# Kernel optimization log

Measured on AMD Instinct MI355X. Metric: run time of the kernel, lower is better.

## Reference

```python
import jax, jax.numpy as jnp
import numpy as np

B, D_FEAT, D_ATTR, N_CLS = 512, 2048, 312, 150


def setup_inputs() -> dict:
    key = jax.random.key(0)
    k1, k2, k3, k4, k5 = jax.random.split(key, 5)
    return {
        "x_f": jax.random.normal(k1, (B, D_FEAT), dtype=jnp.float32),
        "W": jax.random.normal(k2, (D_FEAT, D_ATTR), dtype=jnp.float32) * 0.02,
        "b": jax.random.normal(k3, (D_ATTR,), dtype=jnp.float32) * 0.02,
        "seen_att": jax.random.normal(k4, (N_CLS, D_ATTR), dtype=jnp.float32),
        "x_labels": jax.random.randint(k5, (B,), 0, N_CLS, dtype=jnp.int64),
    }


def reference(x_f, W, b, seen_att, x_labels):
    temp = 1.0
    pre_attr = x_f @ W + b                                # [B, D]
    log_p = jax.nn.log_softmax(pre_attr / temp, axis=-1)  # log pre_attr_softmax
    log_g = jax.nn.log_softmax(seen_att[x_labels] / temp, axis=-1)
    g = jnp.exp(log_g)                                    # gt_attr_softmax [B, D]

    # pairwise KL(target = g_i/g_j || input_logits = log(p_i/p_j)), reduction='sum':
    #   sum_d t * (log t - log_ratio_p)
    t_ratio = g[:, None, :] / g[None, :, :]                               # [B, B, D]
    log_t = log_g[:, None, :] - log_g[None, :, :]                         # [B, B, D]
    log_r = log_p[:, None, :] - log_p[None, :, :]                         # [B, B, D]
    kl = jnp.sum(t_ratio * (log_t - log_r), axis=-1)                      # [B, B]

    same = x_labels[:, None] == x_labels[None, :]
    upper = jnp.triu(jnp.ones((x_labels.shape[0],) * 2, dtype=bool), k=1)
    mask = same & upper

    count = jnp.sum(mask)
    loss = jnp.sum(jnp.where(mask, kl, 0.0))
    return jnp.where(count > 0, loss / count.astype(loss.dtype), loss)
```

## Files before the change

### kernel.cpp

```cpp
#include <hip/hip_runtime.h>
#include <math.h>

#define B      512
#define DF     2048
#define DA     312
#define NTHR   320
#define RT     8
#define KSPLIT 16

__device__ __forceinline__ float wave_max_f(float v) {
  #pragma unroll
  for (int off = 32; off >= 1; off >>= 1)
    v = fmaxf(v, __shfl_down(v, off));
  return v;
}

__device__ __forceinline__ double wave_sum_d(double v) {
  #pragma unroll
  for (int off = 32; off >= 1; off >>= 1)
    v += __shfl_down(v, off);
  return v;
}

__global__ __launch_bounds__(NTHR) void gemm_partial_kernel(
    const float* __restrict__ x_f, const float* __restrict__ W,
    float* __restrict__ part, int KC) {
  const int c    = threadIdx.x;
  const int row0 = blockIdx.x * RT;
  const int k0   = blockIdx.y * KC;

  if (c >= DA) return;

  float acc[RT];
  #pragma unroll
  for (int r = 0; r < RT; ++r) acc[r] = 0.f;

  const float* Wp = W + (size_t)k0 * DA + c;
  const float* xp = x_f + (size_t)row0 * DF + k0;

  for (int k = 0; k < KC; k += 8) {
    float w[8];
    #pragma unroll
    for (int j = 0; j < 8; ++j) w[j] = Wp[(size_t)(k + j) * DA];
    #pragma unroll
    for (int r = 0; r < RT; ++r) {
      const float* xr = xp + (size_t)r * DF + k;
      #pragma unroll
      for (int j = 0; j < 8; ++j) acc[r] = fmaf(xr[j], w[j], acc[r]);
    }
  }

  #pragma unroll
  for (int r = 0; r < RT; ++r)
    part[((size_t)blockIdx.y * B + row0 + r) * DA + c] = acc[r];
}

__global__ __launch_bounds__(NTHR) void row_stats_kernel(
    const float* __restrict__ part, const float* __restrict__ b,
    double* __restrict__ S, int ksplit) {
  __shared__ float  red_f[8];
  __shared__ double red_d[16];
  __shared__ float  bcast_max;

  const int tid  = threadIdx.x;
  const int wid  = tid >> 6;
  const int lane = tid & 63;
  const int row  = blockIdx.x;

  float v = -INFINITY;
  if (tid < DA) {
    float s = b[tid];
    for (int p = 0; p < ksplit; ++p)
      s += part[((size_t)p * B + row) * DA + tid];
    v = s;
  }

  float m = wave_max_f(v);
  if (lane == 0) red_f[wid] = m;
  __syncthreads();
  if (tid == 0) {
    float mm = red_f[0];
    #pragma unroll
    for (int w = 1; w < NTHR / 64; ++w) mm = fmaxf(mm, red_f[w]);
    bcast_max = mm;
  }
  __syncthreads();
  const float rowmax = bcast_max;

  double e  = (tid < DA) ? exp((double)v - (double)rowmax) : 0.0;
  double sp = (tid < DA) ? (double)v : 0.0;
  double es = wave_sum_d(e);
  double ss = wave_sum_d(sp);
  if (lane == 0) { red_d[wid] = es; red_d[8 + wid] = ss; }
  __syncthreads();
  if (tid == 0) {
    double esum = 0.0, ssum = 0.0;
    #pragma unroll
    for (int w = 0; w < NTHR / 64; ++w) { esum += red_d[w]; ssum += red_d[8 + w]; }
    S[row] = ssum - (double)DA * ((double)rowmax + log(esum));
  }
}

__global__ __launch_bounds__(1024) void pair_reduce_kernel(
    const double* __restrict__ S, const int* __restrict__ labels,
    float* __restrict__ out) {
  __shared__ double    Ss[B];
  __shared__ int       Ls[B];
  __shared__ double    red_d[16];
  __shared__ long long red_i[16];

  const int tid = threadIdx.x;
  if (tid < B) { Ss[tid] = S[tid]; Ls[tid] = labels[tid]; }
  __syncthreads();

  double lsum = 0.0;
  long long lcnt = 0;
  for (int p = tid; p < B * B; p += 1024) {
    int i = p >> 9;
    int j = p & (B - 1);
    if (j > i && Ls[i] == Ls[j]) { lsum += Ss[j] - Ss[i]; lcnt++; }
  }

  #pragma unroll
  for (int off = 32; off >= 1; off >>= 1) {
    lsum += __shfl_down(lsum, off);
    lcnt += __shfl_down(lcnt, off);
  }
  const int wid = tid >> 6, lane = tid & 63;
  if (lane == 0) { red_d[wid] = lsum; red_i[wid] = lcnt; }
  __syncthreads();
  if (tid == 0) {
    double s = 0.0; long long c = 0;
    #pragma unroll
    for (int w = 0; w < 16; ++w) { s += red_d[w]; c += red_i[w]; }
    out[0] = (float)((c > 0) ? s / (double)c : s);
  }
}

extern "C" void kernel_launch(void* const* d_in, const int* in_sizes, int n_in,
                              void* d_out, int out_size, void* d_ws, size_t ws_size,
                              hipStream_t stream) {
  const float* x_f    = (const float*)d_in[0];
  const float* W      = (const float*)d_in[1];
  const float* b      = (const float*)d_in[2];
  const int*   labels = (const int*)d_in[4];

  int ksplit = KSPLIT;
  if (ws_size < (size_t)KSPLIT * B * DA * 4 + 8192) ksplit = 2;

  float*  part = (float*)d_ws;
  size_t  part_bytes = ((size_t)ksplit * B * DA * 4 + 255) & ~(size_t)255;
  double* S    = (double*)((char*)d_ws + part_bytes);
  const int KC = DF / ksplit;

  dim3 g1(B / RT, ksplit);
  gemm_partial_kernel<<<g1, NTHR, 0, stream>>>(x_f, W, part, KC);
  row_stats_kernel<<<B, NTHR, 0, stream>>>(part, b, S, ksplit);
  pair_reduce_kernel<<<1, 1024, 0, stream>>>(S, labels, (float*)d_out);
}
```

Baseline: 113.4 us.

## Fuse GEMM, row stats and pair reduction into one kernel via atomic tickets

Merges the three kernels into a single launch. The last split-K block for each row group, chosen by an atomic ticket counter, reduces the partials and computes the row log-softmax statistics. The last row-group finisher then does the pairwise label reduction. This removes two kernel launches and their inter-kernel gaps at the cost of a memset, atomics, threadfences, and the serial row-stats and pair tail running on only a few blocks with 320 threads.

```diff
diff --git a/kernel.cpp b/kernel.cpp
--- a/kernel.cpp
+++ b/kernel.cpp
@@ -7,6 +7,7 @@
 #define NTHR   320
 #define RT     8
 #define KSPLIT 16
+#define NRG    (B / RT)
 
 __device__ __forceinline__ float wave_max_f(float v) {
   #pragma unroll
@@ -22,118 +23,132 @@
   return v;
 }
 
-__global__ __launch_bounds__(NTHR) void gemm_partial_kernel(
+__global__ __launch_bounds__(NTHR) void fused_kernel(
     const float* __restrict__ x_f, const float* __restrict__ W,
-    float* __restrict__ part, int KC) {
+    const float* __restrict__ b, const int* __restrict__ labels,
+    float* __restrict__ part, double* __restrict__ S,
+    int* counters, float* __restrict__ out,
+    int ksplit, int KC) {
   const int c    = threadIdx.x;
-  const int row0 = blockIdx.x * RT;
-  const int k0   = blockIdx.y * KC;
+  const int rg   = blockIdx.x;
+  const int ks   = blockIdx.y;
+  const int row0 = rg * RT;
+  const int k0   = ks * KC;
 
-  if (c >= DA) return;
+  __shared__ int       ticket_sh;
+  __shared__ float     red_f[8];
+  __shared__ float     bcast_max;
+  __shared__ double    red_d[16];
+  __shared__ long long red_i[8];
+  __shared__ double    Ss[B];
+  __shared__ int       Ls[B];
 
-  float acc[RT];
-  #pragma unroll
-  for (int r = 0; r < RT; ++r) acc[r] = 0.f;
+  if (c < DA) {
+    float acc[RT];
+    #pragma unroll
+    for (int r = 0; r < RT; ++r) acc[r] = 0.f;
 
-  const float* Wp = W + (size_t)k0 * DA + c;
-  const float* xp = x_f + (size_t)row0 * DF + k0;
+    const float* Wp = W + (size_t)k0 * DA + c;
+    const float* xp = x_f + (size_t)row0 * DF + k0;
 
-  for (int k = 0; k < KC; k += 8) {
-    float w[8];
+    for (int k = 0; k < KC; k += 8) {
+      float w[8];
+      #pragma unroll
+      for (int j = 0; j < 8; ++j) w[j] = Wp[(size_t)(k + j) * DA];
+      #pragma unroll
+      for (int r = 0; r < RT; ++r) {
+        const float* xr = xp + (size_t)r * DF + k;
+        #pragma unroll
+        for (int j = 0; j < 8; ++j) acc[r] = fmaf(xr[j], w[j], acc[r]);
+      }
+    }
+
+    float* pp = part + (size_t)(rg * ksplit + ks) * RT * DA + c;
     #pragma unroll
-    for (int j = 0; j < 8; ++j) w[j] = Wp[(size_t)(k + j) * DA];
+    for (int r = 0; r < RT; ++r) pp[(size_t)r * DA] = acc[r];
+  }
+
+  __threadfence();
+  if (threadIdx.x == 0)
+    ticket_sh = atomicAdd(&counters[rg], 1);
+  __syncthreads();
+  if (ticket_sh != ksplit - 1) return;
+  __threadfence();
+
+  const int wid  = threadIdx.x >> 6;
+  const int lane = threadIdx.x & 63;
+
+  float s[RT];
+  if (c < DA) {
+    const float bias = b[c];
     #pragma unroll
-    for (int r = 0; r < RT; ++r) {
-      const float* xr = xp + (size_t)r * DF + k;
+    for (int r = 0; r < RT; ++r) s[r] = bias;
+    const float* pb = part + (size_t)rg * ksplit * RT * DA + c;
+    for (int p = 0; p < ksplit; ++p) {
       #pragma unroll
-      for (int j = 0; j < 8; ++j) acc[r] = fmaf(xr[j], w[j], acc[r]);
+      for (int r = 0; r < RT; ++r)
+        s[r] += pb[((size_t)p * RT + r) * DA];
     }
   }
 
-  #pragma unroll
-  for (int r = 0; r < RT; ++r)
-    part[((size_t)blockIdx.y * B + row0 + r) * DA + c] = acc[r];
-}
+  for (int r = 0; r < RT; ++r) {
+    float v = (c < DA) ? s[r] : -INFINITY;
+    float m = wave_max_f(v);
+    if (lane == 0) red_f[wid] = m;
+    __syncthreads();
+    if (threadIdx.x == 0) {
+      float mm = red_f[0];
+      #pragma unroll
+      for (int w = 1; w < NTHR / 64; ++w) mm = fmaxf(mm, red_f[w]);
+      bcast_max = mm;
+    }
+    __syncthreads();
+    const float rowmax = bcast_max;
 
-__global__ __launch_bounds__(NTHR) void row_stats_kernel(
-    const float* __restrict__ part, const float* __restrict__ b,
-    double* __restrict__ S, int ksplit) {
-  __shared__ float  red_f[8];
-  __shared__ double red_d[16];
-  __shared__ float  bcast_max;
-
-  const int tid  = threadIdx.x;
-  const int wid  = tid >> 6;
-  const int lane = tid & 63;
-  const int row  = blockIdx.x;
-
-  float v = -INFINITY;
-  if (tid < DA) {
-    float s = b[tid];
-    for (int p = 0; p < ksplit; ++p)
-      s += part[((size_t)p * B + row) * DA + tid];
-    v = s;
+    double e  = (c < DA) ? exp((double)v - (double)rowmax) : 0.0;
+    double sp = (c < DA) ? (double)v : 0.0;
+    double es = wave_sum_d(e);
+    double ss = wave_sum_d(sp);
+    if (lane == 0) { red_d[wid] = es; red_d[8 + wid] = ss; }
+    __syncthreads();
+    if (threadIdx.x == 0) {
+      double esum = 0.0, ssum = 0.0;
+      #pragma unroll
+      for (int w = 0; w < NTHR / 64; ++w) { esum += red_d[w]; ssum += red_d[8 + w]; }
+      S[row0 + r] = ssum - (double)DA * ((double)rowmax + log(esum));
+    }
+    __syncthreads();
   }
 
-  float m = wave_max_f(v);
-  if (lane == 0) red_f[wid] = m;
+  __threadfence();
+  if (threadIdx.x == 0)
+    ticket_sh = atomicAdd(&counters[NRG], 1);
   __syncthreads();
-  if (tid == 0) {
-    float mm = red_f[0];
-    #pragma unroll
-    for (int w = 1; w < NTHR / 64; ++w) mm = fmaxf(mm, red_f[w]);
-    bcast_max = mm;
-  }
-  __syncthreads();
-  const float rowmax = bcast_max;
+  if (ticket_sh != NRG - 1) return;
+  __threadfence();
 
-  double e  = (tid < DA) ? exp((double)v - (double)rowmax) : 0.0;
-  double sp = (tid < DA) ? (double)v : 0.0;
-  double es = wave_sum_d(e);
-  double ss = wave_sum_d(sp);
-  if (lane == 0) { red_d[wid] = es; red_d[8 + wid] = ss; }
-  __syncthreads();
-  if (tid == 0) {
-    double esum = 0.0, ssum = 0.0;
-    #pragma unroll
-    for (int w = 0; w < NTHR / 64; ++w) { esum += red_d[w]; ssum += red_d[8 + w]; }
-    S[row] = ssum - (double)DA * ((double)rowmax + log(esum));
-  }
-}
-
-__global__ __launch_bounds__(1024) void pair_reduce_kernel(
-    const double* __restrict__ S, const int* __restrict__ labels,
-    float* __restrict__ out) {
-  __shared__ double    Ss[B];
-  __shared__ int       Ls[B];
-  __shared__ double    red_d[16];
-  __shared__ long long red_i[16];
-
-  const int tid = threadIdx.x;
-  if (tid < B) { Ss[tid] = S[tid]; Ls[tid] = labels[tid]; }
+  for (int i = threadIdx.x; i < B; i += NTHR) { Ss[i] = S[i]; Ls[i] = labels[i]; }
   __syncthreads();
 
   double lsum = 0.0;
   long long lcnt = 0;
-  for (int p = tid; p < B * B; p += 1024) {
+  for (int p = threadIdx.x; p < B * B; p += NTHR) {
     int i = p >> 9;
     int j = p & (B - 1);
     if (j > i && Ls[i] == Ls[j]) { lsum += Ss[j] - Ss[i]; lcnt++; }
   }
-
   #pragma unroll
   for (int off = 32; off >= 1; off >>= 1) {
     lsum += __shfl_down(lsum, off);
     lcnt += __shfl_down(lcnt, off);
   }
-  const int wid = tid >> 6, lane = tid & 63;
   if (lane == 0) { red_d[wid] = lsum; red_i[wid] = lcnt; }
   __syncthreads();
-  if (tid == 0) {
-    double s = 0.0; long long c = 0;
+  if (threadIdx.x == 0) {
+    double s2 = 0.0; long long c2 = 0;
     #pragma unroll
-    for (int w = 0; w < 16; ++w) { s += red_d[w]; c += red_i[w]; }
-    out[0] = (float)((c > 0) ? s / (double)c : s);
+    for (int w = 0; w < NTHR / 64; ++w) { s2 += red_d[w]; c2 += red_i[w]; }
+    out[0] = (float)((c2 > 0) ? s2 / (double)c2 : s2);
   }
 }
 
@@ -146,15 +161,16 @@
   const int*   labels = (const int*)d_in[4];
 
   int ksplit = KSPLIT;
-  if (ws_size < (size_t)KSPLIT * B * DA * 4 + 8192) ksplit = 2;
+  size_t need = 8192 + (size_t)KSPLIT * B * DA * 4;
+  if (ws_size < need) ksplit = 2;
 
-  float*  part = (float*)d_ws;
-  size_t  part_bytes = ((size_t)ksplit * B * DA * 4 + 255) & ~(size_t)255;
-  double* S    = (double*)((char*)d_ws + part_bytes);
+  int*    counters = (int*)d_ws;
+  double* S        = (double*)((char*)d_ws + 512);
+  float*  part     = (float*)((char*)d_ws + 8192);
   const int KC = DF / ksplit;
 
-  dim3 g1(B / RT, ksplit);
-  gemm_partial_kernel<<<g1, NTHR, 0, stream>>>(x_f, W, part, KC);
-  row_stats_kernel<<<B, NTHR, 0, stream>>>(part, b, S, ksplit);
-  pair_reduce_kernel<<<1, 1024, 0, stream>>>(S, labels, (float*)d_out);
+  hipMemsetAsync(d_ws, 0, 512, stream);
+  dim3 g(NRG, ksplit);
+  fused_kernel<<<g, NTHR, 0, stream>>>(x_f, W, b, labels, part, S, counters,
+                                       (float*)d_out, ksplit, KC);
 }
```

Result: slower. 309.7 us (+173.1%).
